# Kernel tuning notes

Hardware: AMD Instinct MI355X
Metric: run time of the kernel (lower is better)

The kernel has to match this reference:

```python
import jax, jax.numpy as jnp
import numpy as np

N_NODES = 20000
N_EDGES = 640000
N_TRIP = 1000000
C = 128          # channels
E = 64           # expansion_features
CUTOFF = 5.0
LOG2 = float(np.log(2.0))


def ssp(x):
    # ShiftedSoftplus
    return jax.nn.softplus(x) - LOG2


def setup_inputs() -> dict:
    key = jax.random.key(0)
    ks = jax.random.split(key, 12)
    features = jax.random.normal(ks[0], (N_NODES, C), dtype=jnp.float32)
    neighbour_distances = jax.random.uniform(ks[1], (N_EDGES,), dtype=jnp.float32) * (1.2 * CUTOFF)
    neighbour_list = jax.random.randint(ks[2], (2, N_EDGES), 0, N_NODES, dtype=jnp.int32)
    triplet_idxs = jax.random.randint(ks[3], (N_TRIP, 3), 0, N_NODES, dtype=jnp.int32)
    angles = jax.random.uniform(ks[4], (N_TRIP,), dtype=jnp.float32) * np.pi
    r_ij = jax.random.uniform(ks[5], (N_TRIP,), dtype=jnp.float32) * CUTOFF
    r_ik = jax.random.uniform(ks[6], (N_TRIP,), dtype=jnp.float32) * CUTOFF
    # learned parameters (Linear layers without bias; stored [in, out])
    W_pre = jax.random.normal(ks[7], (C, C), dtype=jnp.float32) / np.sqrt(C)
    W2b1 = jax.random.normal(ks[8], (E, E), dtype=jnp.float32) / np.sqrt(E)
    W2b2 = jax.random.normal(ks[9], (E, C), dtype=jnp.float32) / np.sqrt(E)
    W3b1 = jax.random.normal(ks[10], (3, C // 2), dtype=jnp.float32) / np.sqrt(3.0)
    W3b2 = jax.random.normal(ks[11], (C // 2, C), dtype=jnp.float32) / np.sqrt(C // 2)
    W_post = jax.random.normal(jax.random.fold_in(key, 99), (C, C), dtype=jnp.float32) / np.sqrt(C)
    return {
        "features": features,
        "neighbour_distances": neighbour_distances,
        "neighbour_list": neighbour_list,
        "triplet_idxs": triplet_idxs,
        "angles": angles,
        "r_ij": r_ij,
        "r_ik": r_ik,
        "W_pre": W_pre,
        "W2b1": W2b1,
        "W2b2": W2b2,
        "W3b1": W3b1,
        "W3b2": W3b2,
        "W_post": W_post,
    }


def reference(features, neighbour_distances, neighbour_list, triplet_idxs,
              angles, r_ij, r_ik, W_pre, W2b1, W2b2, W3b1, W3b2, W_post):
    # 1) pre-linear
    h = features @ W_pre                                   # [N, C]

    # 2) radial basis (Gaussian smearing) with smooth cosine cutoff envelope
    centers = jnp.linspace(0.0, CUTOFF, E, dtype=jnp.float32)  # [E]
    width = CUTOFF / E
    gamma = 1.0 / (2.0 * width * width)
    d = neighbour_distances[:, None]                       # [n_edges, 1]
    rb = jnp.exp(-gamma * (d - centers) ** 2)              # [n_edges, E]
    cutoff_mask = (neighbour_distances < CUTOFF).astype(jnp.float32)
    cutoff_values = 0.5 * (1.0 + jnp.cos(np.pi * neighbour_distances / CUTOFF))
    rb = rb * (cutoff_values * cutoff_mask)[:, None]       # fused envelope

    # 3) two-body messages: gather neighbour node features, modulate by radial MLP
    neighbor_h = h[neighbour_list[1]]                      # [n_edges, C]
    two_body = neighbor_h * (ssp(rb @ W2b1) @ W2b2)        # [n_edges, C]

    # 4) three-body messages: angular MLP on (r_ij, r_ik, cos(angle)),
    #    gather node features at triplet_idxs[:,1], scatter-add into edge slots
    tbf = jnp.stack([r_ij, r_ik, jnp.cos(angles)], axis=-1)  # [n_trip, 3]
    w3 = ssp(tbf @ W3b1) @ W3b2                              # [n_trip, C]
    msgs = h[triplet_idxs[:, 1]] * w3                        # [n_trip, C]
    edge_msgs = jnp.zeros_like(two_body).at[triplet_idxs[:, 1]].add(msgs)

    # 5) aggregate messages over neighbours (to central atom = neighbour_list[0])
    messages = two_body + edge_msgs
    agg = jax.ops.segment_sum(messages, neighbour_list[0], num_segments=N_NODES)

    # 6) post-linear
    return agg @ W_post
```

## Files before the change

kernel.cpp:

```cpp
#include <hip/hip_runtime.h>
#include <hip/hip_fp16.h>
#include <math.h>

#define TID threadIdx.x

typedef ushort u16x8 __attribute__((ext_vector_type(8)));
typedef unsigned char uchar;

static constexpr int NN = 20000;
static constexpr int NE = 640000;
static constexpr int NT = 1000000;
static constexpr int C = 128;
static constexpr int E = 64;
static constexpr int LUTN = 4104;
static constexpr int NBKT = 313;
static constexpr int NB2 = 512;
static constexpr int CHE2 = 1250;
static constexpr int CHT2 = 1954;
static constexpr int G_GEMM = (NN + 15) / 16;
static constexpr int G_LUT = (LUTN + 7) / 8 + 1;
static constexpr int G_CONS_E = 1024;
static constexpr int G_CONS_T = 1024;
static constexpr float CUT = 5.0f;
static constexpr float LN2 = 0.69314718055994530942f;

__device__ __forceinline__ float ssp(float x) {
    return fmaxf(x, 0.0f) + __logf(1.0f + __expf(-fabsf(x))) - LN2;
}

__device__ __forceinline__ ushort f2bf(float x) {
    uint u = __float_as_uint(x);
    return (ushort)((u + 0x7FFFu + ((u >> 16) & 1u)) >> 16);
}

__device__ __forceinline__ float bf2f(ushort u) {
    return __uint_as_float((uint)u << 16);
}

__device__ __forceinline__ float h2f(uint bits) {
    return __half2float(__ushort_as_half((ushort)(bits & 0xFFFFu)));
}

__global__ __launch_bounds__(256) void k_front(const float* __restrict__ features,
                                               const float* __restrict__ W_pre,
                                               ushort* __restrict__ hB,
                                               const float* __restrict__ W2b1,
                                               const float* __restrict__ W2b2,
                                               ushort* __restrict__ lutB,
                                               float2* __restrict__ spLut,
                                               const int* __restrict__ nl0,
                                               const int* __restrict__ tidx,
                                               uchar* __restrict__ cntE,
                                               uchar* __restrict__ cntT) {
    __shared__ __align__(16) char smem[53248];
    const int bid = blockIdx.x;
    if (bid < G_GEMM) {
        ushort* wB = (ushort*)smem;
        float (*aL)[132] = (float(*)[132])(smem + 32768);
        for (int i = TID; i < C * C / 4; i += 256) {
            float4 w4 = ((const float4*)W_pre)[i];
            ushort4 u = {f2bf(w4.x), f2bf(w4.y), f2bf(w4.z), f2bf(w4.w)};
            ((ushort4*)wB)[i] = u;
        }
        const int base = bid * 16;
        for (int i = TID; i < 512; i += 256) {
            int r = base + (i >> 5);
            float4 v = (r < NN) ? ((const float4*)features)[(size_t)r * 32 + (i & 31)]
                                : (float4){0.f, 0.f, 0.f, 0.f};
            *(float4*)&aL[i >> 5][(i & 31) << 2] = v;
        }
        __syncthreads();
        const int rg = TID >> 4;
        const int c8 = (TID & 15) << 3;
        float acc[8] = {0.f, 0.f, 0.f, 0.f, 0.f, 0.f, 0.f, 0.f};
        #pragma unroll 8
        for (int k = 0; k < C; ++k) {
            float a = aL[rg][k];
            u16x8 wv = *(const u16x8*)&wB[k * C + c8];
            #pragma unroll
            for (int j = 0; j < 8; ++j) acc[j] = fmaf(a, bf2f(wv[j]), acc[j]);
        }
        int r = base + rg;
        if (r < NN) {
            u16x8 u;
            #pragma unroll
            for (int j = 0; j < 8; ++j) u[j] = f2bf(acc[j]);
            *(u16x8*)&hB[(size_t)r * C + c8] = u;
        }
        return;
    }
    if (bid < G_GEMM + G_LUT) {
        const int lb = bid - G_GEMM;
        if (lb == G_LUT - 1) {
            for (int e = TID; e < 512; e += 256) {
                float t0 = (float)e * (1.0f / 32.0f);
                float t1 = (float)(e + 1) * (1.0f / 32.0f);
                float v0 = log1pf(__expf(-t0));
                float v1 = log1pf(__expf(-t1));
                spLut[e] = make_float2(v0, v1 - v0);
            }
            return;
        }
        float* w1 = (float*)smem;
        float* w2 = (float*)(smem + 16384);
        float (*rbL)[E] = (float(*)[E])(smem + 49152);
        float (*hid)[E] = (float(*)[E])(smem + 51200);
        for (int i = TID; i < E * E; i += 256) w1[i] = W2b1[i];
        for (int i = TID; i < E * C; i += 256) w2[i] = W2b2[i];
        const int jj = TID & 63;
        const int esA = TID >> 6;
        const int eg = TID >> 5;
        const int c4 = (TID & 31) << 2;
        const float gamma = 81.92f;
        const float cstep = CUT / 63.0f;
        const float delta = CUT / 4096.0f;
        const int base = lb * 8;
        __syncthreads();
        #pragma unroll
        for (int s = 0; s < 2; ++s) {
            int es = esA + 4 * s;
            float d = (float)(base + es) * delta;
            float cv = (d < CUT) ? 0.5f * (1.0f + __cosf((float)M_PI * d / CUT)) : 0.0f;
            float dd = d - (float)jj * cstep;
            rbL[es][jj] = __expf(-gamma * dd * dd) * cv;
        }
        __syncthreads();
        #pragma unroll
        for (int s = 0; s < 2; ++s) {
            int es = esA + 4 * s;
            float a = 0.f;
            #pragma unroll 16
            for (int k = 0; k < E; ++k)
                a = fmaf(rbL[es][k], w1[k * E + jj], a);
            hid[es][jj] = ssp(a);
        }
        __syncthreads();
        float4 o = {0.f, 0.f, 0.f, 0.f};
        #pragma unroll
        for (int j = 0; j < E; ++j) {
            float t = hid[eg][j];
            const float4 w4 = *(const float4*)&w2[j * C + c4];
            o.x = fmaf(t, w4.x, o.x);
            o.y = fmaf(t, w4.y, o.y);
            o.z = fmaf(t, w4.z, o.z);
            o.w = fmaf(t, w4.w, o.w);
        }
        int row = base + eg;
        if (row < LUTN) {
            ushort4 u = {f2bf(o.x), f2bf(o.y), f2bf(o.z), f2bf(o.w)};
            *(ushort4*)&lutB[(size_t)row * C + c4] = u;
        }
        return;
    }
    {
        int* h = (int*)smem;
        const int b = bid - G_GEMM - G_LUT;
        for (int i = TID; i < NBKT; i += 256) h[i] = 0;
        __syncthreads();
        const int e0 = b * CHE2, e1 = min(e0 + CHE2, NE);
        for (int i = e0 + TID; i < e1; i += 256) atomicAdd(&h[nl0[i] >> 6], 1);
        __syncthreads();
        for (int i = TID; i < NBKT; i += 256) { cntE[(size_t)i * NB2 + b] = (uchar)h[i]; h[i] = 0; }
        __syncthreads();
        const int t0 = b * CHT2, t1 = min(t0 + CHT2, NT);
        for (int i = t0 + TID; i < t1; i += 256) atomicAdd(&h[tidx[3 * i + 1] >> 6], 1);
        __syncthreads();
        for (int i = TID; i < NBKT; i += 256) cntT[(size_t)i * NB2 + b] = (uchar)h[i];
    }
}

__global__ __launch_bounds__(256) void k_bscan(const uchar* __restrict__ cE,
                                               const uchar* __restrict__ cT,
                                               ushort* __restrict__ baseE,
                                               ushort* __restrict__ baseT,
                                               int* __restrict__ totEb,
                                               int* __restrict__ totTb) {
    const int lane = TID & 63;
    const int wv = TID >> 6;
    int task = blockIdx.x * 4 + wv;
    if (task >= 2 * NBKT) return;
    const bool isE = task < NBKT;
    const int k = isE ? task : task - NBKT;
    const uchar* src = isE ? cE : cT;
    ushort* dst = isE ? baseE : baseT;
    int* dT = isE ? totEb : totTb;
    int v[8], pre[8], s = 0;
    #pragma unroll
    for (int j = 0; j < 8; ++j) {
        v[j] = src[(size_t)k * NB2 + lane * 8 + j];
        pre[j] = s;
        s += v[j];
    }
    int incl = s;
    #pragma unroll
    for (int off = 1; off < 64; off <<= 1) {
        int t = __shfl_up(incl, off, 64);
        if (lane >= off) incl += t;
    }
    int excl = incl - s;
    #pragma unroll
    for (int j = 0; j < 8; ++j)
        dst[(size_t)k * NB2 + lane * 8 + j] = (ushort)(excl + pre[j]);
    if (lane == 63) dT[k] = incl;
}

__device__ void scan_one(const int* __restrict__ hist, int* __restrict__ start, int n) {
    __shared__ int wsum[16];
    __shared__ int carryS;
    const int lane = TID & 63;
    const int wv = TID >> 6;
    if (TID == 0) carryS = 0;
    __syncthreads();
    for (int base = 0; base < n; base += 1024) {
        int i = base + TID;
        int v = (i < n) ? hist[i] : 0;
        int acc = v;
        #pragma unroll
        for (int off = 1; off < 64; off <<= 1) {
            int t = __shfl_up(acc, off, 64);
            if (lane >= off) acc += t;
        }
        if (lane == 63) wsum[wv] = acc;
        __syncthreads();
        int woff = 0;
        for (int w = 0; w < wv; ++w) woff += wsum[w];
        int excl = carryS + woff + acc - v;
        if (i < n) start[i] = excl;
        __syncthreads();
        if (TID == 1023) carryS = excl + v;
        __syncthreads();
    }
}

__global__ __launch_bounds__(1024) void k_bktscan(const int* __restrict__ totEb, int* __restrict__ bksE,
                                                  const int* __restrict__ totTb, int* __restrict__ bksT) {
    if (blockIdx.x == 0) scan_one(totEb, bksE, NBKT);
    else                 scan_one(totTb, bksT, NBKT);
}

__global__ __launch_bounds__(256) void k_bplace(const int* __restrict__ nl0,
                                                const int* __restrict__ nl1,
                                                const float* __restrict__ dist,
                                                const int* __restrict__ tidx,
                                                const float* __restrict__ angles,
                                                const float* __restrict__ rij,
                                                const float* __restrict__ rik,
                                                const ushort* __restrict__ baseE,
                                                const ushort* __restrict__ baseT,
                                                const int* __restrict__ bksE,
                                                const int* __restrict__ bksT,
                                                int2* __restrict__ eT,
                                                int2* __restrict__ tT) {
    __shared__ int cur[NBKT];
    const int b = blockIdx.x;
    for (int k = TID; k < NBKT; k += 256)
        cur[k] = bksE[k] + (int)baseE[(size_t)k * NB2 + b];
    __syncthreads();
    const int e0 = b * CHE2, e1 = min(e0 + CHE2, NE);
    for (int i = e0 + TID; i < e1; i += 256) {
        int n0 = nl0[i];
        int pos = atomicAdd(&cur[n0 >> 6], 1);
        uint tq = (uint)fmaf(dist[i], 209715.2f, 0.5f);
        eT[pos] = make_int2((int)(tq | ((uint)(n0 & 63) << 26)), nl1[i]);
    }
    __syncthreads();
    for (int k = TID; k < NBKT; k += 256)
        cur[k] = bksT[k] + (int)baseT[(size_t)k * NB2 + b];
    __syncthreads();
    const int t0 = b * CHT2, tEnd = min(t0 + CHT2, NT);
    for (int i = t0 + TID; i < tEnd; i += 256) {
        int t1 = tidx[3 * i + 1];
        int pos = atomicAdd(&cur[t1 >> 6], 1);
        uint ab = ((uint)__half_as_ushort(__float2half_rn(rik[i])) << 16)
                | (uint)__half_as_ushort(__float2half_rn(rij[i]));
        uint cc = (uint)__half_as_ushort(__float2half_rn(__cosf(angles[i])))
                | ((uint)(t1 & 63) << 16);
        tT[pos] = make_int2((int)ab, (int)cc);
    }
}

__global__ __launch_bounds__(256) void k_nsort(const int2* __restrict__ eTs,
                                               const int2* __restrict__ tTs,
                                               const int* __restrict__ bksE,
                                               const int* __restrict__ bksT,
                                               const int* __restrict__ totEb,
                                               const int* __restrict__ totTb,
                                               int2* __restrict__ eS,
                                               int2* __restrict__ tS,
                                               int* __restrict__ startE,
                                               int* __restrict__ totE,
                                               int* __restrict__ startT,
                                               int* __restrict__ totT) {
    __shared__ int hist[64];
    __shared__ int cur[64];
    const bool isE = blockIdx.x < NBKT;
    const int bkt = isE ? blockIdx.x : blockIdx.x - NBKT;
    const int2* src = isE ? eTs : tTs;
    int2* dst = isE ? eS : tS;
    const int s0 = isE ? bksE[bkt] : bksT[bkt];
    const int cnt = isE ? totEb[bkt] : totTb[bkt];
    int* stX = isE ? startE : startT;
    int* ttX = isE ? totE : totT;
    if (TID < 64) hist[TID] = 0;
    __syncthreads();
    for (int i = TID; i < cnt; i += 256) {
        int2 p = src[s0 + i];
        int nlo = isE ? (int)(((uint)p.x >> 26) & 63u) : (int)(((uint)p.y >> 16) & 63u);
        atomicAdd(&hist[nlo], 1);
    }
    __syncthreads();
    if (TID < 64) {
        int v = hist[TID];
        int incl = v;
        #pragma unroll
        for (int off = 1; off < 64; off <<= 1) {
            int t = __shfl_up(incl, off, 64);
            if (TID >= off) incl += t;
        }
        int excl = incl - v;
        cur[TID] = s0 + excl;
        int node = bkt * 64 + TID;
        if (node < NN) { stX[node] = s0 + excl; ttX[node] = v; }
    }
    __syncthreads();
    for (int i = TID; i < cnt; i += 256) {
        int2 p = src[s0 + i];
        int nlo = isE ? (int)(((uint)p.x >> 26) & 63u) : (int)(((uint)p.y >> 16) & 63u);
        int pos = atomicAdd(&cur[nlo], 1);
        dst[pos] = p;
    }
}

__global__ __launch_bounds__(256) void k_consume(const int2* __restrict__ eS,
                                                 const int* __restrict__ startE,
                                                 const int* __restrict__ totE,
                                                 const ushort* __restrict__ hB,
                                                 const ushort* __restrict__ lutB,
                                                 float* __restrict__ agg,
                                                 const int2* __restrict__ tS,
                                                 const int* __restrict__ startT,
                                                 const int* __restrict__ totT,
                                                 const float* __restrict__ W3b1,
                                                 const float2* __restrict__ spLut,
                                                 float* __restrict__ uacc) {
    __shared__ __align__(16) char smem[10752];
    const int lane = TID & 63;
    const int wv = TID >> 6;
    if (blockIdx.x < G_CONS_E) {
        int4 (*stage)[2][64] = (int4(*)[2][64])smem;
        const int c2b = lane << 2;
        for (int r = blockIdx.x * 4 + wv; r < NN; r += G_CONS_E * 4) {
            const int s0 = startE[r];
            const int cnt = totE[r];
            float a0 = 0.f, a1 = 0.f;
            int2 pf;
            if (lane < min(64, cnt)) pf = eS[s0 + lane];
            const int nch = (cnt + 63) >> 6;
            for (int c = 0; c < nch; ++c) {
                const int base = c << 6;
                const int n = min(64, cnt - base);
                const int slot = c & 1;
                if (lane < n) {
                    uint tq = ((uint)pf.x) & 0x03FFFFFFu;
                    int idx = min((int)(tq >> 8), LUTN - 2);
                    float fr = (float)(tq & 255u) * (1.0f / 256.0f);
                    stage[wv][slot][lane] = make_int4(idx * (C * 2), __float_as_int(fr),
                                                      pf.y * (C * 2), 0);
                }
                int nb = base + 64;
                if (nb < cnt && lane < cnt - nb) pf = eS[s0 + nb + lane];
                asm volatile("s_waitcnt lgkmcnt(0)" ::: "memory");
                #pragma unroll 8
                for (int i = 0; i < n; ++i) {
                    int4 q = stage[wv][slot][i];
                    float fr = __int_as_float(q.y);
                    ushort2 A2 = *(const ushort2*)((const char*)lutB + q.x + c2b);
                    ushort2 B2 = *(const ushort2*)((const char*)lutB + q.x + 256 + c2b);
                    ushort2 H2 = *(const ushort2*)((const char*)hB + q.z + c2b);
                    float ax = bf2f(A2.x), ay = bf2f(A2.y);
                    float ox = fmaf(fr, bf2f(B2.x) - ax, ax);
                    float oy = fmaf(fr, bf2f(B2.y) - ay, ay);
                    a0 = fmaf(ox, bf2f(H2.x), a0);
                    a1 = fmaf(oy, bf2f(H2.y), a1);
                }
            }
            asm volatile("s_waitcnt lgkmcnt(0)" ::: "memory");
            float2 o = {a0, a1};
            *(float2*)&agg[(size_t)r * C + (lane << 1)] = o;
        }
        return;
    }
    {
        uint* spl = (uint*)smem;
        float4 (*stage)[2][64] = (float4(*)[2][64])(smem + 2048);
        for (int i = TID; i < 512; i += 256) {
            float2 vs = spLut[i];
            spl[i] = ((uint)f2bf(vs.y) << 16) | (uint)f2bf(vs.x);
        }
        __syncthreads();
        const float w1a = W3b1[lane];
        const float w1b = W3b1[64 + lane];
        const float w1c = W3b1[128 + lane];
        const int bid = blockIdx.x - G_CONS_E;
        for (int r = bid * 4 + wv; r < NN; r += G_CONS_T * 4) {
            const int s0 = startT[r];
            const int cnt = totT[r];
            float usA = 0.f, usB = 0.f;
            uint2 pf;
            if (lane < min(64, cnt)) pf = ((const uint2*)tS)[s0 + lane];
            const int nch = (cnt + 63) >> 6;
            for (int c = 0; c < nch; ++c) {
                const int base = c << 6;
                const int n = min(64, cnt - base);
                const int slot = c & 1;
                if (lane < n) {
                    float4 f;
                    f.x = h2f(pf.x);
                    f.y = h2f(pf.x >> 16);
                    f.z = h2f(pf.y);
                    f.w = 0.f;
                    stage[wv][slot][lane] = f;
                }
                int nb = base + 64;
                if (nb < cnt && lane < cnt - nb) pf = ((const uint2*)tS)[s0 + nb + lane];
                asm volatile("s_waitcnt lgkmcnt(0)" ::: "memory");
                int i = 0;
                #pragma unroll 4
                for (; i + 1 < n; i += 2) {
                    float4 pa = stage[wv][slot][i];
                    float4 pb = stage[wv][slot][i + 1];
                    float xa = fmaf(pa.x, w1a, fmaf(pa.y, w1b, pa.z * w1c));
                    float xb = fmaf(pb.x, w1a, fmaf(pb.y, w1b, pb.z * w1c));
                    float ta = fabsf(xa) * 32.0f;
                    float tb = fabsf(xb) * 32.0f;
                    int ia = min((int)ta, 511);
                    int ib = min((int)tb, 511);
                    float fa = ta - (float)ia;
                    float fb = tb - (float)ib;
                    uint va = spl[ia];
                    uint vb = spl[ib];
                    usA += fmaxf(xa, 0.f) + fmaf(fa, bf2f((ushort)(va >> 16)), bf2f((ushort)va));
                    usB += fmaxf(xb, 0.f) + fmaf(fb, bf2f((ushort)(vb >> 16)), bf2f((ushort)vb));
                }
                if (i < n) {
                    float4 pa = stage[wv][slot][i];
                    float xa = fmaf(pa.x, w1a, fmaf(pa.y, w1b, pa.z * w1c));
                    float ta = fabsf(xa) * 32.0f;
                    int ia = min((int)ta, 511);
                    float fa = ta - (float)ia;
                    uint va = spl[ia];
                    usA += fmaxf(xa, 0.f) + fmaf(fa, bf2f((ushort)(va >> 16)), bf2f((ushort)va));
                }
            }
            asm volatile("s_waitcnt lgkmcnt(0)" ::: "memory");
            uacc[(size_t)r * 64 + lane] = usA + usB - LN2 * (float)cnt;
        }
    }
}

__global__ __launch_bounds__(256) void k_node_final(const float* __restrict__ uacc,
                                                    const float* __restrict__ W3b2,
                                                    const ushort* __restrict__ hB,
                                                    const int* __restrict__ nl0,
                                                    float* __restrict__ agg) {
    __shared__ uint w2p[64 * 64];
    __shared__ float uL[16][68];
    for (int i = TID; i < 4096; i += 256) {
        int k = i >> 6, l = i & 63;
        w2p[i] = ((uint)f2bf(W3b2[k * C + 64 + l]) << 16) | (uint)f2bf(W3b2[k * C + l]);
    }
    const int base = blockIdx.x * 16;
    {
        int i = TID;
        int row = i >> 4, col = (i & 15) << 2;
        float4 v = ((const float4*)uacc)[(size_t)(base + row) * 16 + (i & 15)];
        *(float4*)&uL[row][col] = v;
    }
    __syncthreads();
    const int lane = TID & 63;
    const int wv = TID >> 6;
    #pragma unroll
    for (int j = 0; j < 4; ++j) {
        const int row = wv * 4 + j;
        float o0 = 0.f, o1 = 0.f;
        #pragma unroll 8
        for (int k = 0; k < 64; ++k) {
            float a = uL[row][k];
            uint wp = w2p[k * 64 + lane];
            o0 = fmaf(a, __uint_as_float(wp << 16), o0);
            o1 = fmaf(a, __uint_as_float(wp & 0xFFFF0000u), o1);
        }
        const int r = base + row;
        const int n0 = nl0[r];
        float h0 = bf2f(hB[(size_t)r * C + lane]);
        float h1 = bf2f(hB[(size_t)r * C + 64 + lane]);
        unsafeAtomicAdd(&agg[(size_t)n0 * C + lane], o0 * h0);
        unsafeAtomicAdd(&agg[(size_t)n0 * C + 64 + lane], o1 * h1);
    }
}

__global__ __launch_bounds__(256) void k_gemm16f(const float* __restrict__ A,
                                                 const float* __restrict__ W,
                                                 float* __restrict__ out, int nrows) {
    __shared__ ushort wB[C * C];
    __shared__ float aL[16][132];
    for (int i = TID; i < C * C / 4; i += 256) {
        float4 w4 = ((const float4*)W)[i];
        ushort4 u = {f2bf(w4.x), f2bf(w4.y), f2bf(w4.z), f2bf(w4.w)};
        ((ushort4*)wB)[i] = u;
    }
    const int base = blockIdx.x * 16;
    for (int i = TID; i < 512; i += 256) {
        int r = base + (i >> 5);
        float4 v = (r < nrows) ? ((const float4*)A)[(size_t)r * 32 + (i & 31)]
                               : (float4){0.f, 0.f, 0.f, 0.f};
        *(float4*)&aL[i >> 5][(i & 31) << 2] = v;
    }
    __syncthreads();
    const int rg = TID >> 4;
    const int c8 = (TID & 15) << 3;
    float acc[8] = {0.f, 0.f, 0.f, 0.f, 0.f, 0.f, 0.f, 0.f};
    #pragma unroll 8
    for (int k = 0; k < C; ++k) {
        float a = aL[rg][k];
        u16x8 wv = *(const u16x8*)&wB[k * C + c8];
        #pragma unroll
        for (int j = 0; j < 8; ++j) acc[j] = fmaf(a, bf2f(wv[j]), acc[j]);
    }
    int r = base + rg;
    if (r < nrows) {
        float4 o0 = {acc[0], acc[1], acc[2], acc[3]};
        float4 o1 = {acc[4], acc[5], acc[6], acc[7]};
        *(float4*)&out[(size_t)r * C + c8] = o0;
        *(float4*)&out[(size_t)r * C + c8 + 4] = o1;
    }
}

extern "C" void kernel_launch(void* const* d_in, const int* in_sizes, int n_in,
                              void* d_out, int out_size, void* d_ws, size_t ws_size,
                              hipStream_t stream) {
    const float* features = (const float*)d_in[0];
    const float* ndist    = (const float*)d_in[1];
    const int*   nlist    = (const int*)d_in[2];
    const int*   tidx     = (const int*)d_in[3];
    const float* angles   = (const float*)d_in[4];
    const float* rij      = (const float*)d_in[5];
    const float* rik      = (const float*)d_in[6];
    const float* W_pre    = (const float*)d_in[7];
    const float* W2b1     = (const float*)d_in[8];
    const float* W2b2     = (const float*)d_in[9];
    const float* W3b1     = (const float*)d_in[10];
    const float* W3b2     = (const float*)d_in[11];
    const float* W_post   = (const float*)d_in[12];
    float* out = (float*)d_out;

    char* w = (char*)d_ws;
    float* agg    = (float*)w;
    int2* eT      = (int2*)w;
    w += (size_t)NN * C * 4;
    ushort* hB    = (ushort*)w;  w += (size_t)NN * C * 2;
    ushort* lutB  = (ushort*)w;  w += (size_t)LUTN * C * 2;
    int2* eS      = (int2*)w;    w += (size_t)NE * 8;
    int2* tS      = (int2*)w;    w += (size_t)NT * 8;
    int2* tT      = (int2*)w;
    float* uacc   = (float*)w;
    w += (size_t)NT * 8;
    uchar* cntE   = (uchar*)w;   w += (size_t)NBKT * NB2;
    uchar* cntT   = (uchar*)w;   w += (size_t)NBKT * NB2;
    ushort* baseE = (ushort*)w;  w += (size_t)NBKT * NB2 * 2;
    ushort* baseT = (ushort*)w;  w += (size_t)NBKT * NB2 * 2;
    int* totEb    = (int*)w;     w += 1280;
    int* totTb    = (int*)w;     w += 1280;
    int* bksE     = (int*)w;     w += 1280;
    int* bksT     = (int*)w;     w += 1280;
    int* startE   = (int*)w;     w += (size_t)NN * 4;
    int* totE     = (int*)w;     w += (size_t)NN * 4;
    int* startT   = (int*)w;     w += (size_t)NN * 4;
    int* totT     = (int*)w;     w += (size_t)NN * 4;
    float2* spLut = (float2*)w;  w += 512 * 8;

    const int* nl0 = nlist;
    const int* nl1 = nlist + NE;

    hipLaunchKernelGGL(k_front, dim3(G_GEMM + G_LUT + NB2), dim3(256), 0, stream,
                       features, W_pre, hB, W2b1, W2b2, lutB, spLut,
                       nl0, tidx, cntE, cntT);
    hipLaunchKernelGGL(k_bscan, dim3((2 * NBKT + 3) / 4), dim3(256), 0, stream,
                       cntE, cntT, baseE, baseT, totEb, totTb);
    hipLaunchKernelGGL(k_bktscan, dim3(2), dim3(1024), 0, stream,
                       totEb, bksE, totTb, bksT);
    hipLaunchKernelGGL(k_bplace, dim3(NB2), dim3(256), 0, stream,
                       nl0, nl1, ndist, tidx, angles, rij, rik,
                       baseE, baseT, bksE, bksT, eT, tT);
    hipLaunchKernelGGL(k_nsort, dim3(2 * NBKT), dim3(256), 0, stream,
                       eT, tT, bksE, bksT, totEb, totTb,
                       eS, tS, startE, totE, startT, totT);
    hipLaunchKernelGGL(k_consume, dim3(G_CONS_E + G_CONS_T), dim3(256), 0, stream,
                       eS, startE, totE, hB, lutB, agg,
                       tS, startT, totT, W3b1, spLut, uacc);
    hipLaunchKernelGGL(k_node_final, dim3(NN / 16), dim3(256), 0, stream,
                       uacc, W3b2, hB, nl0, agg);
    hipLaunchKernelGGL(k_gemm16f, dim3((NN + 15) / 16), dim3(256), 0, stream,
                       agg, W_post, out, NN);
}
```

Before: 175.4 us.

## Fold bucket scan into consumers and pre-pack LUT with interpolation deltas

Removes the separate single-block bucket-total scan kernel. Each k_bplace and k_nsort block now redoes that 313-element prefix scan in shared memory from the bucket totals. The radial LUT is repacked into an interleaved (value, delta) bf16 layout in a new pass merged into the base-scan kernel. The edge consumer can then fetch both interpolation endpoints with one 8-byte load instead of two 4-byte loads and skip a subtraction. The costs are redundant scans in every block, an extra LUT-sized buffer, and rounding of the deltas to bf16.

Result: slower. 183.0 us (+4.3%).

```diff
diff --git a/kernel.cpp b/kernel.cpp
--- a/kernel.cpp
+++ b/kernel.cpp
@@ -19,6 +19,8 @@
 static constexpr int CHT2 = 1954;
 static constexpr int G_GEMM = (NN + 15) / 16;
 static constexpr int G_LUT = (LUTN + 7) / 8 + 1;
+static constexpr int G_SCAN = (2 * NBKT + 3) / 4;
+static constexpr int G_PACK = LUTN / 8;
 static constexpr int G_CONS_E = 1024;
 static constexpr int G_CONS_T = 1024;
 static constexpr float CUT = 5.0f;
@@ -169,12 +171,31 @@
     }
 }
 
-__global__ __launch_bounds__(256) void k_bscan(const uchar* __restrict__ cE,
-                                               const uchar* __restrict__ cT,
-                                               ushort* __restrict__ baseE,
-                                               ushort* __restrict__ baseT,
-                                               int* __restrict__ totEb,
-                                               int* __restrict__ totTb) {
+__global__ __launch_bounds__(256) void k_mid(const uchar* __restrict__ cE,
+                                             const uchar* __restrict__ cT,
+                                             ushort* __restrict__ baseE,
+                                             ushort* __restrict__ baseT,
+                                             int* __restrict__ totEb,
+                                             int* __restrict__ totTb,
+                                             const ushort* __restrict__ lutB,
+                                             ushort* __restrict__ lutP) {
+    if (blockIdx.x >= G_SCAN) {
+        const int pb = blockIdx.x - G_SCAN;
+        for (int i = TID; i < 8 * 64; i += 256) {
+            int idx = pb * 8 + (i >> 6);
+            int cp = i & 63;
+            int idx1 = min(idx + 1, LUTN - 1);
+            ushort2 v = *(const ushort2*)&lutB[(size_t)idx * C + cp * 2];
+            ushort2 n = *(const ushort2*)&lutB[(size_t)idx1 * C + cp * 2];
+            ushort4 o;
+            o.x = v.x;
+            o.y = f2bf(bf2f(n.x) - bf2f(v.x));
+            o.z = v.y;
+            o.w = f2bf(bf2f(n.y) - bf2f(v.y));
+            *(ushort4*)&lutP[((size_t)idx * 64 + cp) * 4] = o;
+        }
+        return;
+    }
     const int lane = TID & 63;
     const int wv = TID >> 6;
     int task = blockIdx.x * 4 + wv;
@@ -204,40 +225,6 @@
     if (lane == 63) dT[k] = incl;
 }
 
-__device__ void scan_one(const int* __restrict__ hist, int* __restrict__ start, int n) {
-    __shared__ int wsum[16];
-    __shared__ int carryS;
-    const int lane = TID & 63;
-    const int wv = TID >> 6;
-    if (TID == 0) carryS = 0;
-    __syncthreads();
-    for (int base = 0; base < n; base += 1024) {
-        int i = base + TID;
-        int v = (i < n) ? hist[i] : 0;
-        int acc = v;
-        #pragma unroll
-        for (int off = 1; off < 64; off <<= 1) {
-            int t = __shfl_up(acc, off, 64);
-            if (lane >= off) acc += t;
-        }
-        if (lane == 63) wsum[wv] = acc;
-        __syncthreads();
-        int woff = 0;
-        for (int w = 0; w < wv; ++w) woff += wsum[w];
-        int excl = carryS + woff + acc - v;
-        if (i < n) start[i] = excl;
-        __syncthreads();
-        if (TID == 1023) carryS = excl + v;
-        __syncthreads();
-    }
-}
-
-__global__ __launch_bounds__(1024) void k_bktscan(const int* __restrict__ totEb, int* __restrict__ bksE,
-                                                  const int* __restrict__ totTb, int* __restrict__ bksT) {
-    if (blockIdx.x == 0) scan_one(totEb, bksE, NBKT);
-    else                 scan_one(totTb, bksT, NBKT);
-}
-
 __global__ __launch_bounds__(256) void k_bplace(const int* __restrict__ nl0,
                                                 const int* __restrict__ nl1,
                                                 const float* __restrict__ dist,
@@ -247,14 +234,36 @@
                                                 const float* __restrict__ rik,
                                                 const ushort* __restrict__ baseE,
                                                 const ushort* __restrict__ baseT,
-                                                const int* __restrict__ bksE,
-                                                const int* __restrict__ bksT,
+                                                const int* __restrict__ totEb,
+                                                const int* __restrict__ totTb,
                                                 int2* __restrict__ eT,
                                                 int2* __restrict__ tT) {
     __shared__ int cur[NBKT];
+    __shared__ int bksEs[NBKT];
+    __shared__ int bksTs[NBKT];
+    const int lane = TID & 63;
+    const int wv = TID >> 6;
+    if (wv < 2) {
+        const int* tot = (wv == 0) ? totEb : totTb;
+        int* dst = (wv == 0) ? bksEs : bksTs;
+        int carry = 0;
+        for (int b2 = 0; b2 < NBKT; b2 += 64) {
+            int idx = b2 + lane;
+            int vv = (idx < NBKT) ? tot[idx] : 0;
+            int incl = vv;
+            #pragma unroll
+            for (int off = 1; off < 64; off <<= 1) {
+                int t = __shfl_up(incl, off, 64);
+                if (lane >= off) incl += t;
+            }
+            if (idx < NBKT) dst[idx] = carry + incl - vv;
+            carry += __shfl(incl, 63, 64);
+        }
+    }
+    __syncthreads();
     const int b = blockIdx.x;
     for (int k = TID; k < NBKT; k += 256)
-        cur[k] = bksE[k] + (int)baseE[(size_t)k * NB2 + b];
+        cur[k] = bksEs[k] + (int)baseE[(size_t)k * NB2 + b];
     __syncthreads();
     const int e0 = b * CHE2, e1 = min(e0 + CHE2, NE);
     for (int i = e0 + TID; i < e1; i += 256) {
@@ -265,7 +274,7 @@
     }
     __syncthreads();
     for (int k = TID; k < NBKT; k += 256)
-        cur[k] = bksT[k] + (int)baseT[(size_t)k * NB2 + b];
+        cur[k] = bksTs[k] + (int)baseT[(size_t)k * NB2 + b];
     __syncthreads();
     const int t0 = b * CHT2, tEnd = min(t0 + CHT2, NT);
     for (int i = t0 + TID; i < tEnd; i += 256) {
@@ -281,8 +290,6 @@
 
 __global__ __launch_bounds__(256) void k_nsort(const int2* __restrict__ eTs,
                                                const int2* __restrict__ tTs,
-                                               const int* __restrict__ bksE,
-                                               const int* __restrict__ bksT,
                                                const int* __restrict__ totEb,
                                                const int* __restrict__ totTb,
                                                int2* __restrict__ eS,
@@ -293,16 +300,35 @@
                                                int* __restrict__ totT) {
     __shared__ int hist[64];
     __shared__ int cur[64];
+    __shared__ int bksS[NBKT];
     const bool isE = blockIdx.x < NBKT;
     const int bkt = isE ? blockIdx.x : blockIdx.x - NBKT;
     const int2* src = isE ? eTs : tTs;
     int2* dst = isE ? eS : tS;
-    const int s0 = isE ? bksE[bkt] : bksT[bkt];
-    const int cnt = isE ? totEb[bkt] : totTb[bkt];
+    const int* totB = isE ? totEb : totTb;
     int* stX = isE ? startE : startT;
     int* ttX = isE ? totE : totT;
+    const int lane = TID & 63;
+    const int wv = TID >> 6;
+    if (wv == 0) {
+        int carry = 0;
+        for (int b2 = 0; b2 < NBKT; b2 += 64) {
+            int idx = b2 + lane;
+            int vv = (idx < NBKT) ? totB[idx] : 0;
+            int incl = vv;
+            #pragma unroll
+            for (int off = 1; off < 64; off <<= 1) {
+                int t = __shfl_up(incl, off, 64);
+                if (lane >= off) incl += t;
+            }
+            if (idx < NBKT) bksS[idx] = carry + incl - vv;
+            carry += __shfl(incl, 63, 64);
+        }
+    }
     if (TID < 64) hist[TID] = 0;
     __syncthreads();
+    const int s0 = bksS[bkt];
+    const int cnt = totB[bkt];
     for (int i = TID; i < cnt; i += 256) {
         int2 p = src[s0 + i];
         int nlo = isE ? (int)(((uint)p.x >> 26) & 63u) : (int)(((uint)p.y >> 16) & 63u);
@@ -335,7 +361,7 @@
                                                  const int* __restrict__ startE,
                                                  const int* __restrict__ totE,
                                                  const ushort* __restrict__ hB,
-                                                 const ushort* __restrict__ lutB,
+                                                 const ushort* __restrict__ lutP,
                                                  float* __restrict__ agg,
                                                  const int2* __restrict__ tS,
                                                  const int* __restrict__ startT,
@@ -348,6 +374,7 @@
     const int wv = TID >> 6;
     if (blockIdx.x < G_CONS_E) {
         int4 (*stage)[2][64] = (int4(*)[2][64])smem;
+        const int c8b = lane << 3;
         const int c2b = lane << 2;
         for (int r = blockIdx.x * 4 + wv; r < NN; r += G_CONS_E * 4) {
             const int s0 = startE[r];
@@ -364,7 +391,7 @@
                     uint tq = ((uint)pf.x) & 0x03FFFFFFu;
                     int idx = min((int)(tq >> 8), LUTN - 2);
                     float fr = (float)(tq & 255u) * (1.0f / 256.0f);
-                    stage[wv][slot][lane] = make_int4(idx * (C * 2), __float_as_int(fr),
+                    stage[wv][slot][lane] = make_int4(idx << 9, __float_as_int(fr),
                                                       pf.y * (C * 2), 0);
                 }
                 int nb = base + 64;
@@ -374,12 +401,10 @@
                 for (int i = 0; i < n; ++i) {
                     int4 q = stage[wv][slot][i];
                     float fr = __int_as_float(q.y);
-                    ushort2 A2 = *(const ushort2*)((const char*)lutB + q.x + c2b);
-                    ushort2 B2 = *(const ushort2*)((const char*)lutB + q.x + 256 + c2b);
+                    ushort4 P = *(const ushort4*)((const char*)lutP + q.x + c8b);
                     ushort2 H2 = *(const ushort2*)((const char*)hB + q.z + c2b);
-                    float ax = bf2f(A2.x), ay = bf2f(A2.y);
-                    float ox = fmaf(fr, bf2f(B2.x) - ax, ax);
-                    float oy = fmaf(fr, bf2f(B2.y) - ay, ay);
+                    float ox = fmaf(fr, bf2f(P.y), bf2f(P.x));
+                    float oy = fmaf(fr, bf2f(P.w), bf2f(P.z));
                     a0 = fmaf(ox, bf2f(H2.x), a0);
                     a1 = fmaf(oy, bf2f(H2.y), a1);
                 }
@@ -560,6 +585,7 @@
     w += (size_t)NN * C * 4;
     ushort* hB    = (ushort*)w;  w += (size_t)NN * C * 2;
     ushort* lutB  = (ushort*)w;  w += (size_t)LUTN * C * 2;
+    ushort* lutP  = (ushort*)w;  w += (size_t)LUTN * C * 4;
     int2* eS      = (int2*)w;    w += (size_t)NE * 8;
     int2* tS      = (int2*)w;    w += (size_t)NT * 8;
     int2* tT      = (int2*)w;
@@ -571,8 +597,6 @@
     ushort* baseT = (ushort*)w;  w += (size_t)NBKT * NB2 * 2;
     int* totEb    = (int*)w;     w += 1280;
     int* totTb    = (int*)w;     w += 1280;
-    int* bksE     = (int*)w;     w += 1280;
-    int* bksT     = (int*)w;     w += 1280;
     int* startE   = (int*)w;     w += (size_t)NN * 4;
     int* totE     = (int*)w;     w += (size_t)NN * 4;
     int* startT   = (int*)w;     w += (size_t)NN * 4;
@@ -585,18 +609,16 @@
     hipLaunchKernelGGL(k_front, dim3(G_GEMM + G_LUT + NB2), dim3(256), 0, stream,
                        features, W_pre, hB, W2b1, W2b2, lutB, spLut,
                        nl0, tidx, cntE, cntT);
-    hipLaunchKernelGGL(k_bscan, dim3((2 * NBKT + 3) / 4), dim3(256), 0, stream,
-                       cntE, cntT, baseE, baseT, totEb, totTb);
-    hipLaunchKernelGGL(k_bktscan, dim3(2), dim3(1024), 0, stream,
-                       totEb, bksE, totTb, bksT);
+    hipLaunchKernelGGL(k_mid, dim3(G_SCAN + G_PACK), dim3(256), 0, stream,
+                       cntE, cntT, baseE, baseT, totEb, totTb, lutB, lutP);
     hipLaunchKernelGGL(k_bplace, dim3(NB2), dim3(256), 0, stream,
                        nl0, nl1, ndist, tidx, angles, rij, rik,
-                       baseE, baseT, bksE, bksT, eT, tT);
+                       baseE, baseT, totEb, totTb, eT, tT);
     hipLaunchKernelGGL(k_nsort, dim3(2 * NBKT), dim3(256), 0, stream,
-                       eT, tT, bksE, bksT, totEb, totTb,
+                       eT, tT, totEb, totTb,
                        eS, tS, startE, totE, startT, totT);
     hipLaunchKernelGGL(k_consume, dim3(G_CONS_E + G_CONS_T), dim3(256), 0, stream,
-                       eS, startE, totE, hB, lutB, agg,
+                       eS, startE, totE, hB, lutP, agg,
                        tS, startT, totT, W3b1, spLut, uacc);
     hipLaunchKernelGGL(k_node_final, dim3(NN / 16), dim3(256), 0, stream,
                        uacc, W3b2, hB, nl0, agg);
```
